# Optimization experiments

Measured on AMD Instinct MI355X. Metric: run time of the kernel, lower is better.

## Reference

```python
import jax, jax.numpy as jnp
import numpy as np
from jax import lax

B = 1024       # number of subgraphs (unique batch ids)
L = 64         # max_seq_len
CIN = 512
COUT = 512
K = 3
SEG = 48       # nodes per subgraph (uniform, <= L)
N = B * SEG
EPS = 1e-5


def setup_inputs() -> dict:
    key = jax.random.key(0)
    k1, k2 = jax.random.split(key, 2)
    x = jax.random.normal(k1, (N, CIN), jnp.float32)
    # sorted segment ids, every id 0..B-1 present (as graph_to_nn_batch assumes)
    batch = (jnp.arange(N) // SEG).astype(jnp.int32)
    conv_w = jax.random.normal(k2, (COUT, CIN, K), jnp.float32) * 0.02
    conv_b = jnp.zeros((COUT,), jnp.float32)
    gamma = jnp.ones((COUT,), jnp.float32)
    beta = jnp.zeros((COUT,), jnp.float32)
    return {"x": x, "batch": batch, "conv_w": conv_w, "conv_b": conv_b,
            "gamma": gamma, "beta": beta}


def _gather_pad(x, batch):
    # position of each node within its segment (batch is sorted)
    n = x.shape[0]
    pos = jnp.arange(n) - jnp.searchsorted(batch, batch)  # first-occurrence offset
    keep = pos < L                                        # truncate overflow rows
    pos_c = jnp.minimum(pos, L - 1)
    xm = jnp.where(keep[:, None], x, jnp.zeros((), x.dtype))
    dense = jnp.zeros((B, L, x.shape[1]), x.dtype).at[batch, pos_c].add(xm)
    return dense.transpose(0, 2, 1)  # [B, C, L]


def reference(x, batch, conv_w, conv_b, gamma, beta):
    dense = _gather_pad(x, batch)                              # [B, CIN, L]
    out = lax.conv_general_dilated(
        dense, conv_w, window_strides=(1,), padding=[(1, 1)],
        dimension_numbers=("NCH", "OIH", "NCH"))               # [B, COUT, L]
    out = out + conv_b[None, :, None]
    # BatchNorm (training-mode batch statistics over batch+length per channel)
    mean = out.mean(axis=(0, 2))
    var = out.var(axis=(0, 2))
    out = (out - mean[None, :, None]) * lax.rsqrt(var + EPS)[None, :, None]
    out = out * gamma[None, :, None] + beta[None, :, None]
    out = jax.nn.relu(out)                                     # dropout = identity (eval)
    # nn_batch_to_graph: permute(1,0,2).reshape(C,-1).T -> [B*L, COUT]
    out_x = out.transpose(1, 0, 2).reshape(COUT, -1).T
    batch_out = (jnp.arange(B * L) // L).astype(jnp.int32)
    return out_x, batch_out
```

## Files before the change

### kernel.cpp

```cpp
#include <hip/hip_runtime.h>
#include <hip/hip_bf16.h>

#define NB 1024
#define CIN_ 512
#define COUT_ 512
#define SEG_ 48
#define NROWS (NB * 64)
#define EPS_ 1e-5f

typedef __attribute__((ext_vector_type(8))) short bf8;
typedef __attribute__((ext_vector_type(8))) unsigned short u16x8;
typedef __attribute__((ext_vector_type(4))) float f4;

__device__ __forceinline__ unsigned short f2bf(float f) {
    unsigned int u = __float_as_uint(f);
    u += 0x7fffu + ((u >> 16) & 1u);
    return (unsigned short)(u >> 16);
}

__global__ void prep_x(const float* __restrict__ x, unsigned short* __restrict__ xb) {
    int t = blockIdx.x * 256 + threadIdx.x;
    int p  = t & 63;
    int ks = (t >> 6) & 15;
    int b  = t >> 10;
    u16x8 out[4];
    if (p >= 1 && p <= 48) {
        const f4* src = reinterpret_cast<const f4*>(x + ((size_t)(b * SEG_ + p - 1)) * CIN_ + ks * 32);
        #pragma unroll
        for (int lk = 0; lk < 4; ++lk) {
            f4 f0 = src[lk * 2], f1 = src[lk * 2 + 1];
            out[lk][0] = f2bf(f0.x); out[lk][1] = f2bf(f0.y);
            out[lk][2] = f2bf(f0.z); out[lk][3] = f2bf(f0.w);
            out[lk][4] = f2bf(f1.x); out[lk][5] = f2bf(f1.y);
            out[lk][6] = f2bf(f1.z); out[lk][7] = f2bf(f1.w);
        }
    } else {
        u16x8 z = {0,0,0,0,0,0,0,0};
        #pragma unroll
        for (int lk = 0; lk < 4; ++lk) out[lk] = z;
    }
    #pragma unroll
    for (int lk = 0; lk < 4; ++lk)
        *reinterpret_cast<u16x8*>(xb + (((size_t)(b * 16 + ks) * 4 + lk) * 512 + p * 8)) = out[lk];
}

__global__ void prep_w(const float* __restrict__ w, unsigned short* __restrict__ wtfb) {
    int i = blockIdx.x * 256 + threadIdx.x;
    int c8  = i & 7;
    int cop = (i >> 3) & 255;
    int lk  = (i >> 11) & 3;
    int ks  = (i >> 13) & 15;
    int rest = i >> 17;
    int ch = rest / 3, s = rest % 3;
    int co = ch * 256 + cop;
    int ci = ks * 32 + lk * 8 + c8;
    wtfb[i] = f2bf(w[((size_t)co * CIN_ + ci) * 3 + s]);
}

template<int S, int MT>
__device__ __forceinline__ void phase_mma(const char* Bb, const char* Aseg,
                                          int lr, int lk, int wc, f4 (&acc)[4][4]) {
    const char* Bp = Bb + (((lk << 8) + (wc << 6) + lr) << 4);
    const char* Ap = Aseg + (((lk << 6) + lr + S) << 4);
    bf8 bb[4], af[MT];
    #pragma unroll
    for (int nt = 0; nt < 4; ++nt) bb[nt] = *reinterpret_cast<const bf8*>(Bp + (nt << 8));
    #pragma unroll
    for (int mt = 0; mt < MT; ++mt) af[mt] = *reinterpret_cast<const bf8*>(Ap + (mt << 8));
    __builtin_amdgcn_s_setprio(1);
    #pragma unroll
    for (int mt = 0; mt < MT; ++mt)
        #pragma unroll
        for (int nt = 0; nt < 4; ++nt)
            acc[mt][nt] = __builtin_amdgcn_mfma_f32_16x16x32_bf16(af[mt], bb[nt], acc[mt][nt], 0, 0, 0);
    __builtin_amdgcn_s_setprio(0);
}

#define BARF() { __builtin_amdgcn_sched_barrier(0); __builtin_amdgcn_s_barrier(); __builtin_amdgcn_sched_barrier(0); }
#define WAITV(n) asm volatile("s_waitcnt vmcnt(" #n ")" ::: "memory")

template<bool BF16OUT>
__global__ __launch_bounds__(512, 4) void conv_mfma(
    const unsigned short* __restrict__ xb,
    const unsigned short* __restrict__ wtfb,
    const float* __restrict__ cb,
    void* __restrict__ vout_,
    float* __restrict__ psum,
    float* __restrict__ psq)
{
    __shared__ unsigned short sh[32768];
    char* shb = (char*)sh;
    char* Bb0 = shb;
    char* Bb1 = shb + 16384;
    char* Bb2 = shb + 32768;
    char* Aab = shb + 49152;

    const int bid = blockIdx.x;
    const int rb = bid >> 1;
    const int ch = bid & 1;
    const int b2 = rb << 1;
    const int tid = threadIdx.x;
    const int lane = tid & 63;
    const int wv = tid >> 6;
    const int lr = lane & 15;
    const int lk = lane >> 4;
    const int wr = wv >> 2;
    const int wc = wv & 3;

    const char* xc = (const char*)xb;
    const char* wcb = (const char*)wtfb + (size_t)ch * 786432;

    auto stB = [&](const char* chunk, char* dst) {
        const char* s0 = chunk + (wv << 11) + (lane << 4);
        char* d0 = dst + (wv << 11);
        __builtin_amdgcn_global_load_lds((const unsigned int*)s0, (unsigned int*)d0, 16, 0, 0);
        __builtin_amdgcn_global_load_lds((const unsigned int*)(s0 + 1024), (unsigned int*)(d0 + 1024), 16, 0, 0);
    };
    auto chunkA = [&](int b, int ks) { return xc + ((size_t)b * 16 + ks) * 4096; };
    auto chunkB = [&](int s, int ks) { return wcb + (size_t)(s * 16 + ks) * 16384; };
    auto stA = [&](int ksn, char* dst) {
        const char* s0 = ((wv < 4) ? chunkA(b2, ksn) + (wv << 10)
                                   : chunkA(b2 + 1, ksn) + ((wv - 4) << 10)) + (lane << 4);
        __builtin_amdgcn_global_load_lds((const unsigned int*)s0, (unsigned int*)(dst + (wv << 10)), 16, 0, 0);
    };

    f4 acc[4][4];
    #pragma unroll
    for (int mt = 0; mt < 4; ++mt)
        #pragma unroll
        for (int nt = 0; nt < 4; ++nt) { f4 z = {0.f,0.f,0.f,0.f}; acc[mt][nt] = z; }

    stA(0, Aab);
    stB(chunkB(0, 0), Bb0);
    stB(chunkB(1, 0), Bb1);

    #pragma unroll 1
    for (int ks = 0; ks < 16; ++ks) {
        const char* Acur = Aab + ((ks & 1) << 13);
        char* Anxt = (ks < 15) ? (Aab + (((ks + 1) & 1) << 13)) : Bb0;
        const char* Aseg = Acur + (wr << 12);
        const int ksn = (ks < 15) ? ks + 1 : 0;

        stB(chunkB(2, ks), Bb2);
        WAITV(4);
        BARF();
        phase_mma<0, 4>(Bb0, Aseg, lr, lk, wc, acc);
        BARF();

        stA(ksn, Anxt);
        stB(chunkB(0, ksn), Bb0);
        WAITV(5);
        BARF();
        phase_mma<1, 3>(Bb1, Aseg, lr, lk, wc, acc);
        BARF();

        stB(chunkB(1, ksn), Bb1);
        WAITV(5);
        BARF();
        phase_mma<2, 3>(Bb2, Aseg, lr, lk, wc, acc);
        BARF();
    }

    asm volatile("s_waitcnt vmcnt(0)" ::: "memory");
    __builtin_amdgcn_s_barrier();

    const int co_base = (ch << 8) + (wc << 6);
    const int seg = b2 + wr;

    if (BF16OUT) {
        unsigned short* tile = sh;
        #pragma unroll
        for (int nt = 0; nt < 4; ++nt) {
            const int co = co_base + (nt << 4) + lr;
            const int cop = (wc << 6) + (nt << 4) + lr;
            const float bias = cb[co];
            float s1 = 0.f, s2 = 0.f;
            #pragma unroll
            for (int mt = 0; mt < 3; ++mt) {
                #pragma unroll
                for (int r = 0; r < 4; ++r) {
                    float v = acc[mt][nt][r] + bias;
                    s1 += v; s2 += v * v;
                    int row = (mt << 4) + (lk << 2) + r;
                    tile[(wr << 14) + (row << 8) + cop] = f2bf(v);
                }
            }
            {
                float v = acc[3][nt][0] + bias;
                if (lk == 0) {
                    s1 += v; s2 += v * v;
                    tile[(wr << 14) + (48 << 8) + cop] = f2bf(v);
                }
            }
            s1 += __shfl_xor(s1, 16);
            s1 += __shfl_xor(s1, 32);
            s2 += __shfl_xor(s2, 16);
            s2 += __shfl_xor(s2, 32);
            if (lk == 0) {
                psum[seg * COUT_ + co] = s1;
                psq[seg * COUT_ + co] = s2;
            }
        }
        __syncthreads();
        unsigned short* voutc = (unsigned short*)vout_;
        for (int i = tid; i < 3136; i += 512) {
            int sseg = (i >= 1568) ? 1 : 0;
            int rem = i - (sseg ? 1568 : 0);
            int row = rem >> 5;
            int c16 = rem & 31;
            u16x8 v = *reinterpret_cast<const u16x8*>(tile + (sseg << 14) + (row << 8) + (c16 << 3));
            *reinterpret_cast<u16x8*>(voutc + ((size_t)(b2 + sseg) * 49 + row) * 512 + (ch << 8) + (c16 << 3)) = v;
        }
    } else {
        float* voutf = (float*)vout_;
        #pragma unroll
        for (int nt = 0; nt < 4; ++nt) {
            const int co = co_base + (nt << 4) + lr;
            const float bias = cb[co];
            float s1 = 0.f, s2 = 0.f;
            #pragma unroll
            for (int mt = 0; mt < 4; ++mt) {
                #pragma unroll
                for (int r = 0; r < 4; ++r) {
                    float v = acc[mt][nt][r] + bias;
                    s1 += v; s2 += v * v;
                    int l = (mt << 4) + (lk << 2) + r;
                    voutf[(((size_t)seg << 6) + l) * COUT_ + co] = v;
                }
            }
            s1 += __shfl_xor(s1, 16);
            s1 += __shfl_xor(s1, 32);
            s2 += __shfl_xor(s2, 16);
            s2 += __shfl_xor(s2, 32);
            if (lk == 0) {
                psum[seg * COUT_ + co] = s1;
                psq[seg * COUT_ + co] = s2;
            }
        }
    }
}

__global__ void reduce1(const float* __restrict__ psum, const float* __restrict__ psq,
                        float* __restrict__ t1, float* __restrict__ t2) {
    int co = threadIdx.x;
    int j = blockIdx.x;
    float s1 = 0.f, s2 = 0.f;
    #pragma unroll
    for (int k = 0; k < 8; ++k) {
        int i = j * 8 + k;
        s1 += psum[i * COUT_ + co];
        s2 += psq[i * COUT_ + co];
    }
    t1[j * COUT_ + co] = s1;
    t2[j * COUT_ + co] = s2;
}

__global__ void reduce2(const float* __restrict__ t1, const float* __restrict__ t2,
                        const float* __restrict__ gamma, const float* __restrict__ beta,
                        const float* __restrict__ cb, float* __restrict__ scsh,
                        int extraRows) {
    int co = threadIdx.x;
    float s1 = 0.f, s2 = 0.f;
    for (int j = 0; j < 128; ++j) {
        s1 += t1[j * COUT_ + co];
        s2 += t2[j * COUT_ + co];
    }
    float bias = cb[co];
    float er = (float)extraRows;
    s1 += er * bias;
    s2 += er * bias * bias;
    float mean = s1 * (1.f / NROWS);
    float var = s2 * (1.f / NROWS) - mean * mean;
    float rstd = rsqrtf(var + EPS_);
    float sc = gamma[co] * rstd;
    scsh[co] = sc;
    scsh[COUT_ + co] = beta[co] - mean * sc;
}

__global__ void bn_relu_real(const unsigned short* __restrict__ vc,
                             const float* __restrict__ scsh, float* __restrict__ out) {
    const int total = NB * 49 * 64;
    for (int i = blockIdx.x * 256 + threadIdx.x; i < total; i += gridDim.x * 256) {
        int b = i / 3136;
        int rem = i - b * 3136;
        int l = rem >> 6;
        int c8 = (rem & 63) << 3;
        u16x8 v = *reinterpret_cast<const u16x8*>(vc + (size_t)i * 8);
        const float* scp = scsh + c8;
        const float* shp = scsh + COUT_ + c8;
        f4 o0, o1;
        #pragma unroll
        for (int e = 0; e < 4; ++e) {
            float f = __uint_as_float(((unsigned int)v[e]) << 16);
            o0[e] = fmaxf(f * scp[e] + shp[e], 0.f);
        }
        #pragma unroll
        for (int e = 0; e < 4; ++e) {
            float f = __uint_as_float(((unsigned int)v[4 + e]) << 16);
            o1[e] = fmaxf(f * scp[4 + e] + shp[4 + e], 0.f);
        }
        float* op = out + (size_t)b * 32768 + l * 512 + c8;
        *reinterpret_cast<f4*>(op) = o0;
        *reinterpret_cast<f4*>(op + 4) = o1;
    }
}

__global__ void bn_fill_const(const float* __restrict__ cb, const float* __restrict__ scsh,
                              float* __restrict__ out) {
    const int total = NB * 15 * 128;
    for (int i = blockIdx.x * 256 + threadIdx.x; i < total; i += gridDim.x * 256) {
        int b = i / 1920;
        int rem = i - b * 1920;
        int l = 49 + (rem >> 7);
        int c4 = (rem & 127) << 2;
        f4 o;
        #pragma unroll
        for (int e = 0; e < 4; ++e) {
            int co = c4 + e;
            o[e] = fmaxf(cb[co] * scsh[co] + scsh[COUT_ + co], 0.f);
        }
        *reinterpret_cast<f4*>(out + (size_t)b * 32768 + l * 512 + c4) = o;
    }
}

__global__ void bn_relu(float* __restrict__ vout, const float* __restrict__ scsh) {
    const size_t total = (size_t)NROWS * COUT_ / 4;
    for (size_t i = (size_t)blockIdx.x * blockDim.x + threadIdx.x; i < total;
         i += (size_t)gridDim.x * blockDim.x) {
        f4 v = reinterpret_cast<f4*>(vout)[i];
        int co = (int)((i << 2) & (COUT_ - 1));
        f4 sc = *reinterpret_cast<const f4*>(scsh + co);
        f4 sh = *reinterpret_cast<const f4*>(scsh + COUT_ + co);
        v.x = fmaxf(v.x * sc.x + sh.x, 0.f);
        v.y = fmaxf(v.y * sc.y + sh.y, 0.f);
        v.z = fmaxf(v.z * sc.z + sh.z, 0.f);
        v.w = fmaxf(v.w * sc.w + sh.w, 0.f);
        reinterpret_cast<f4*>(vout)[i] = v;
    }
}

__global__ void write_batch(float* __restrict__ o) {
    int i = blockIdx.x * 256 + threadIdx.x;
    if (i < NROWS) o[i] = (float)(i >> 6);
}

extern "C" void kernel_launch(void* const* d_in, const int* in_sizes, int n_in,
                              void* d_out, int out_size, void* d_ws, size_t ws_size,
                              hipStream_t stream) {
    const float* x      = (const float*)d_in[0];
    const float* conv_w = (const float*)d_in[2];
    const float* conv_b = (const float*)d_in[3];
    const float* gamma  = (const float*)d_in[4];
    const float* beta   = (const float*)d_in[5];

    float* out = (float*)d_out;
    float* out_batch = out + (size_t)NROWS * COUT_;

    char* ws = (char*)d_ws;
    unsigned short* xb   = (unsigned short*)ws;
    size_t off = (size_t)NB * 16 * 2048 * 2;
    unsigned short* wtfb = (unsigned short*)(ws + off);
    off += (size_t)786432 * 2;
    float* psum = (float*)(ws + off);  off += (size_t)NB * COUT_ * 4;
    float* psq  = (float*)(ws + off);  off += (size_t)NB * COUT_ * 4;
    float* t1   = (float*)(ws + off);  off += (size_t)128 * COUT_ * 4;
    float* t2   = (float*)(ws + off);  off += (size_t)128 * COUT_ * 4;
    float* scsh = (float*)(ws + off);  off += 4096;
    unsigned short* voutc = (unsigned short*)(ws + off);
    const bool use_bf16 = (ws_size >= off + (size_t)NB * 49 * COUT_ * 2);

    hipLaunchKernelGGL(prep_x, dim3(NB * 16 * 64 / 256), dim3(256), 0, stream, x, xb);
    hipLaunchKernelGGL(prep_w, dim3(786432 / 256), dim3(256), 0, stream, conv_w, wtfb);
    if (use_bf16) {
        hipLaunchKernelGGL((conv_mfma<true>), dim3(NB), dim3(512), 0, stream,
                           xb, wtfb, conv_b, (void*)voutc, psum, psq);
        hipLaunchKernelGGL(reduce1, dim3(128), dim3(512), 0, stream, psum, psq, t1, t2);
        hipLaunchKernelGGL(reduce2, dim3(1), dim3(512), 0, stream, t1, t2, gamma, beta,
                           conv_b, scsh, 15360);
        hipLaunchKernelGGL(bn_relu_real, dim3(2048), dim3(256), 0, stream, voutc, scsh, out);
        hipLaunchKernelGGL(bn_fill_const, dim3(2048), dim3(256), 0, stream, conv_b, scsh, out);
    } else {
        hipLaunchKernelGGL((conv_mfma<false>), dim3(NB), dim3(512), 0, stream,
                           xb, wtfb, conv_b, (void*)out, psum, psq);
        hipLaunchKernelGGL(reduce1, dim3(128), dim3(512), 0, stream, psum, psq, t1, t2);
        hipLaunchKernelGGL(reduce2, dim3(1), dim3(512), 0, stream, t1, t2, gamma, beta,
                           conv_b, scsh, 0);
        hipLaunchKernelGGL(bn_relu, dim3(2048), dim3(256), 0, stream, out, scsh);
    }
    hipLaunchKernelGGL(write_batch, dim3(NROWS / 256), dim3(256), 0, stream, out_batch);
}
```

Baseline: 164.8 us.

## Quad-buffer weight tiles in conv pipeline and merge small launches

The conv kernel moves from three fixed weight LDS buffers to a rotating ring of four 16KB slots. Each weight chunk is now prefetched one full phase earlier, with the vmcnt waits raised to match, so global-to-LDS loads overlap more MMA work. The prep_x/prep_w kernels are merged into one launch, and bn_relu_real, bn_fill_const and write_batch are merged into one bn_finish kernel to cut launch overhead. In exchange, LDS per block grows from 64KB to 80KB, which may lower how many blocks fit per CU and so reduce occupancy.

```diff
diff --git a/kernel.cpp b/kernel.cpp
--- a/kernel.cpp
+++ b/kernel.cpp
@@ -18,43 +18,49 @@
     return (unsigned short)(u >> 16);
 }
 
-__global__ void prep_x(const float* __restrict__ x, unsigned short* __restrict__ xb) {
-    int t = blockIdx.x * 256 + threadIdx.x;
-    int p  = t & 63;
-    int ks = (t >> 6) & 15;
-    int b  = t >> 10;
-    u16x8 out[4];
-    if (p >= 1 && p <= 48) {
-        const f4* src = reinterpret_cast<const f4*>(x + ((size_t)(b * SEG_ + p - 1)) * CIN_ + ks * 32);
+#define PREPX_N 1048576
+#define PREPW_N 786432
+__global__ void prep(const float* __restrict__ x, const float* __restrict__ w,
+                     unsigned short* __restrict__ xb, unsigned short* __restrict__ wtfb) {
+    int idx = blockIdx.x * 256 + threadIdx.x;
+    if (idx < PREPX_N) {
+        int t = idx;
+        int p  = t & 63;
+        int ks = (t >> 6) & 15;
+        int b  = t >> 10;
+        u16x8 out[4];
+        if (p >= 1 && p <= 48) {
+            const f4* src = reinterpret_cast<const f4*>(x + ((size_t)(b * SEG_ + p - 1)) * CIN_ + ks * 32);
+            #pragma unroll
+            for (int lk = 0; lk < 4; ++lk) {
+                f4 f0 = src[lk * 2], f1 = src[lk * 2 + 1];
+                out[lk][0] = f2bf(f0.x); out[lk][1] = f2bf(f0.y);
+                out[lk][2] = f2bf(f0.z); out[lk][3] = f2bf(f0.w);
+                out[lk][4] = f2bf(f1.x); out[lk][5] = f2bf(f1.y);
+                out[lk][6] = f2bf(f1.z); out[lk][7] = f2bf(f1.w);
+            }
+        } else {
+            u16x8 z = {0,0,0,0,0,0,0,0};
+            #pragma unroll
+            for (int lk = 0; lk < 4; ++lk) out[lk] = z;
+        }
         #pragma unroll
-        for (int lk = 0; lk < 4; ++lk) {
-            f4 f0 = src[lk * 2], f1 = src[lk * 2 + 1];
-            out[lk][0] = f2bf(f0.x); out[lk][1] = f2bf(f0.y);
-            out[lk][2] = f2bf(f0.z); out[lk][3] = f2bf(f0.w);
-            out[lk][4] = f2bf(f1.x); out[lk][5] = f2bf(f1.y);
-            out[lk][6] = f2bf(f1.z); out[lk][7] = f2bf(f1.w);
-        }
+        for (int lk = 0; lk < 4; ++lk)
+            *reinterpret_cast<u16x8*>(xb + (((size_t)(b * 16 + ks) * 4 + lk) * 512 + p * 8)) = out[lk];
     } else {
-        u16x8 z = {0,0,0,0,0,0,0,0};
-        #pragma unroll
-        for (int lk = 0; lk < 4; ++lk) out[lk] = z;
-    }
-    #pragma unroll
-    for (int lk = 0; lk < 4; ++lk)
-        *reinterpret_cast<u16x8*>(xb + (((size_t)(b * 16 + ks) * 4 + lk) * 512 + p * 8)) = out[lk];
-}
-
-__global__ void prep_w(const float* __restrict__ w, unsigned short* __restrict__ wtfb) {
-    int i = blockIdx.x * 256 + threadIdx.x;
-    int c8  = i & 7;
-    int cop = (i >> 3) & 255;
-    int lk  = (i >> 11) & 3;
-    int ks  = (i >> 13) & 15;
-    int rest = i >> 17;
-    int ch = rest / 3, s = rest % 3;
-    int co = ch * 256 + cop;
-    int ci = ks * 32 + lk * 8 + c8;
-    wtfb[i] = f2bf(w[((size_t)co * CIN_ + ci) * 3 + s]);
+        int i = idx - PREPX_N;
+        if (i < PREPW_N) {
+            int c8  = i & 7;
+            int cop = (i >> 3) & 255;
+            int lk  = (i >> 11) & 3;
+            int ks  = (i >> 13) & 15;
+            int rest = i >> 17;
+            int ch = rest / 3, s = rest % 3;
+            int co = ch * 256 + cop;
+            int ci = ks * 32 + lk * 8 + c8;
+            wtfb[i] = f2bf(w[((size_t)co * CIN_ + ci) * 3 + s]);
+        }
+    }
 }
 
 template<int S, int MT>
@@ -88,12 +94,9 @@
     float* __restrict__ psum,
     float* __restrict__ psq)
 {
-    __shared__ unsigned short sh[32768];
+    __shared__ unsigned short sh[40960];
     char* shb = (char*)sh;
-    char* Bb0 = shb;
-    char* Bb1 = shb + 16384;
-    char* Bb2 = shb + 32768;
-    char* Aab = shb + 49152;
+    char* Aab = shb + 65536;
 
     const int bid = blockIdx.x;
     const int rb = bid >> 1;
@@ -110,6 +113,7 @@
     const char* xc = (const char*)xb;
     const char* wcb = (const char*)wtfb + (size_t)ch * 786432;
 
+    auto Bslot = [&](int s) { return shb + (s << 14); };
     auto stB = [&](const char* chunk, char* dst) {
         const char* s0 = chunk + (wv << 11) + (lane << 4);
         char* d0 = dst + (wv << 11);
@@ -131,33 +135,34 @@
         for (int nt = 0; nt < 4; ++nt) { f4 z = {0.f,0.f,0.f,0.f}; acc[mt][nt] = z; }
 
     stA(0, Aab);
-    stB(chunkB(0, 0), Bb0);
-    stB(chunkB(1, 0), Bb1);
+    stB(chunkB(0, 0), Bslot(0));
+    stB(chunkB(1, 0), Bslot(1));
+    stB(chunkB(2, 0), Bslot(2));
 
     #pragma unroll 1
     for (int ks = 0; ks < 16; ++ks) {
-        const char* Acur = Aab + ((ks & 1) << 13);
-        char* Anxt = (ks < 15) ? (Aab + (((ks + 1) & 1) << 13)) : Bb0;
-        const char* Aseg = Acur + (wr << 12);
         const int ksn = (ks < 15) ? ks + 1 : 0;
-
-        stB(chunkB(2, ks), Bb2);
-        WAITV(4);
-        BARF();
-        phase_mma<0, 4>(Bb0, Aseg, lr, lk, wc, acc);
+        const int b3 = (3 * ks) & 3;
+        const char* Aseg = Aab + ((ks & 1) << 13) + (wr << 12);
+        char* Anxt = Aab + ((ksn & 1) << 13);
+
+        stB(chunkB(0, ksn), Bslot((b3 + 3) & 3));
+        WAITV(6);
+        BARF();
+        phase_mma<0, 4>(Bslot(b3), Aseg, lr, lk, wc, acc);
         BARF();
 
         stA(ksn, Anxt);
-        stB(chunkB(0, ksn), Bb0);
-        WAITV(5);
-        BARF();
-        phase_mma<1, 3>(Bb1, Aseg, lr, lk, wc, acc);
-        BARF();
-
-        stB(chunkB(1, ksn), Bb1);
-        WAITV(5);
-        BARF();
-        phase_mma<2, 3>(Bb2, Aseg, lr, lk, wc, acc);
+        stB(chunkB(1, ksn), Bslot(b3));
+        WAITV(7);
+        BARF();
+        phase_mma<1, 3>(Bslot((b3 + 1) & 3), Aseg, lr, lk, wc, acc);
+        BARF();
+
+        stB(chunkB(2, ksn), Bslot((b3 + 1) & 3));
+        WAITV(7);
+        BARF();
+        phase_mma<2, 3>(Bslot((b3 + 2) & 3), Aseg, lr, lk, wc, acc);
         BARF();
     }
 
@@ -277,49 +282,59 @@
     scsh[COUT_ + co] = beta[co] - mean * sc;
 }
 
-__global__ void bn_relu_real(const unsigned short* __restrict__ vc,
-                             const float* __restrict__ scsh, float* __restrict__ out) {
-    const int total = NB * 49 * 64;
+#define R1_N (NB * 49 * 64)
+#define R2_N (NB * 15 * 128)
+#define R3_N (NROWS / 4)
+__global__ void bn_finish(const unsigned short* __restrict__ vc,
+                          const float* __restrict__ scsh,
+                          const float* __restrict__ cb,
+                          float* __restrict__ out,
+                          float* __restrict__ out_batch) {
+    const int total = R1_N + R2_N + R3_N;
     for (int i = blockIdx.x * 256 + threadIdx.x; i < total; i += gridDim.x * 256) {
-        int b = i / 3136;
-        int rem = i - b * 3136;
-        int l = rem >> 6;
-        int c8 = (rem & 63) << 3;
-        u16x8 v = *reinterpret_cast<const u16x8*>(vc + (size_t)i * 8);
-        const float* scp = scsh + c8;
-        const float* shp = scsh + COUT_ + c8;
-        f4 o0, o1;
-        #pragma unroll
-        for (int e = 0; e < 4; ++e) {
-            float f = __uint_as_float(((unsigned int)v[e]) << 16);
-            o0[e] = fmaxf(f * scp[e] + shp[e], 0.f);
-        }
-        #pragma unroll
-        for (int e = 0; e < 4; ++e) {
-            float f = __uint_as_float(((unsigned int)v[4 + e]) << 16);
-            o1[e] = fmaxf(f * scp[4 + e] + shp[4 + e], 0.f);
-        }
-        float* op = out + (size_t)b * 32768 + l * 512 + c8;
-        *reinterpret_cast<f4*>(op) = o0;
-        *reinterpret_cast<f4*>(op + 4) = o1;
-    }
-}
-
-__global__ void bn_fill_const(const float* __restrict__ cb, const float* __restrict__ scsh,
-                              float* __restrict__ out) {
-    const int total = NB * 15 * 128;
-    for (int i = blockIdx.x * 256 + threadIdx.x; i < total; i += gridDim.x * 256) {
-        int b = i / 1920;
-        int rem = i - b * 1920;
-        int l = 49 + (rem >> 7);
-        int c4 = (rem & 127) << 2;
-        f4 o;
-        #pragma unroll
-        for (int e = 0; e < 4; ++e) {
-            int co = c4 + e;
-            o[e] = fmaxf(cb[co] * scsh[co] + scsh[COUT_ + co], 0.f);
-        }
-        *reinterpret_cast<f4*>(out + (size_t)b * 32768 + l * 512 + c4) = o;
+        if (i < R1_N) {
+            int b = i / 3136;
+            int rem = i - b * 3136;
+            int l = rem >> 6;
+            int c8 = (rem & 63) << 3;
+            u16x8 v = *reinterpret_cast<const u16x8*>(vc + (size_t)i * 8);
+            const float* scp = scsh + c8;
+            const float* shp = scsh + COUT_ + c8;
+            f4 o0, o1;
+            #pragma unroll
+            for (int e = 0; e < 4; ++e) {
+                float f = __uint_as_float(((unsigned int)v[e]) << 16);
+                o0[e] = fmaxf(f * scp[e] + shp[e], 0.f);
+            }
+            #pragma unroll
+            for (int e = 0; e < 4; ++e) {
+                float f = __uint_as_float(((unsigned int)v[4 + e]) << 16);
+                o1[e] = fmaxf(f * scp[4 + e] + shp[4 + e], 0.f);
+            }
+            float* op = out + (size_t)b * 32768 + l * 512 + c8;
+            *reinterpret_cast<f4*>(op) = o0;
+            *reinterpret_cast<f4*>(op + 4) = o1;
+        } else if (i < R1_N + R2_N) {
+            int k = i - R1_N;
+            int b = k / 1920;
+            int rem = k - b * 1920;
+            int l = 49 + (rem >> 7);
+            int c4 = (rem & 127) << 2;
+            f4 o;
+            #pragma unroll
+            for (int e = 0; e < 4; ++e) {
+                int co = c4 + e;
+                o[e] = fmaxf(cb[co] * scsh[co] + scsh[COUT_ + co], 0.f);
+            }
+            *reinterpret_cast<f4*>(out + (size_t)b * 32768 + l * 512 + c4) = o;
+        } else {
+            int k = i - R1_N - R2_N;
+            int e0 = k << 2;
+            f4 o;
+            #pragma unroll
+            for (int e = 0; e < 4; ++e) o[e] = (float)((e0 + e) >> 6);
+            *reinterpret_cast<f4*>(out_batch + e0) = o;
+        }
     }
 }
 
@@ -369,16 +384,16 @@
     unsigned short* voutc = (unsigned short*)(ws + off);
     const bool use_bf16 = (ws_size >= off + (size_t)NB * 49 * COUT_ * 2);
 
-    hipLaunchKernelGGL(prep_x, dim3(NB * 16 * 64 / 256), dim3(256), 0, stream, x, xb);
-    hipLaunchKernelGGL(prep_w, dim3(786432 / 256), dim3(256), 0, stream, conv_w, wtfb);
+    hipLaunchKernelGGL(prep, dim3((PREPX_N + PREPW_N) / 256), dim3(256), 0, stream,
+                       x, conv_w, xb, wtfb);
     if (use_bf16) {
         hipLaunchKernelGGL((conv_mfma<true>), dim3(NB), dim3(512), 0, stream,
                            xb, wtfb, conv_b, (void*)voutc, psum, psq);
         hipLaunchKernelGGL(reduce1, dim3(128), dim3(512), 0, stream, psum, psq, t1, t2);
         hipLaunchKernelGGL(reduce2, dim3(1), dim3(512), 0, stream, t1, t2, gamma, beta,
                            conv_b, scsh, 15360);
-        hipLaunchKernelGGL(bn_relu_real, dim3(2048), dim3(256), 0, stream, voutc, scsh, out);
-        hipLaunchKernelGGL(bn_fill_const, dim3(2048), dim3(256), 0, stream, conv_b, scsh, out);
+        hipLaunchKernelGGL(bn_finish, dim3(4096), dim3(256), 0, stream,
+                           voutc, scsh, conv_b, out, out_batch);
     } else {
         hipLaunchKernelGGL((conv_mfma<false>), dim3(NB), dim3(512), 0, stream,
                            xb, wtfb, conv_b, (void*)out, psum, psq);
@@ -386,6 +401,6 @@
         hipLaunchKernelGGL(reduce2, dim3(1), dim3(512), 0, stream, t1, t2, gamma, beta,
                            conv_b, scsh, 0);
         hipLaunchKernelGGL(bn_relu, dim3(2048), dim3(256), 0, stream, out, scsh);
-    }
-    hipLaunchKernelGGL(write_batch, dim3(NROWS / 256), dim3(256), 0, stream, out_batch);
-}
+        hipLaunchKernelGGL(write_batch, dim3(NROWS / 256), dim3(256), 0, stream, out_batch);
+    }
+}
```

New measurement: 157.6 us. 1.05x faster.
